# Optimization experiments

Hardware: AMD Instinct MI355X
Metric: run time of the kernel (lower is better)

The kernel has to match this reference:

```python
import jax, jax.numpy as jnp
import numpy as np

NUM_CLUSTERS = 5000  # labels.max()+1, fixed statically for jit
B, K, D, N = 256, 64, 2048, 50000
NHID, H2, NCLASS = 512, 256, 2


def setup_inputs() -> dict:
    key = jax.random.key(0)
    ks = jax.random.split(key, 16)
    s = lambda f_in: 1.0 / np.sqrt(f_in)
    return {
        "indexes": jax.random.randint(ks[0], (B,), 0, N),
        "features": jax.random.normal(ks[1], (N, D), dtype=jnp.float32),
        "labels": jax.random.randint(ks[2], (N,), 0, NUM_CLUSTERS),
        "domain": 1,
        "ori_0": 0,
        "ori_knn_neighbor": jax.random.randint(ks[3], (B, K), 0, N),
        "all_pred": jax.random.normal(ks[4], (B, K, NCLASS), dtype=jnp.float32),
        # GraphConv params (L-GCN style: weight [2*in, out])
        "W1": jax.random.normal(ks[5], (2 * D, NHID), jnp.float32) * s(2 * D),
        "b1": jnp.zeros((NHID,), jnp.float32),
        "W2": jax.random.normal(ks[6], (2 * NHID, H2), jnp.float32) * s(2 * NHID),
        "b2": jnp.zeros((H2,), jnp.float32),
        # classifier: Linear(256,256) -> PReLU(256) -> Linear(256,2)
        "Wc1": jax.random.normal(ks[7], (H2, H2), jnp.float32) * s(H2),
        "bc1": jnp.zeros((H2,), jnp.float32),
        "prelu_a": jnp.full((H2,), 0.25, jnp.float32),
        "Wc2": jax.random.normal(ks[8], (H2, NCLASS), jnp.float32) * s(H2),
        "bc2": jnp.zeros((NCLASS,), jnp.float32),
    }


def _gconv(x, A, W, b):
    # MeanAggregator: bmm(A, x); GraphConv: relu(cat([x, Ax]) @ W + b)
    agg = jnp.einsum('bkj,bjd->bkd', A, x)
    cat = jnp.concatenate([x, agg], axis=-1)
    return jax.nn.relu(jnp.einsum('bkd,df->bkf', cat, W) + b)


def reference(indexes, features, labels, domain, ori_0, ori_knn_neighbor, all_pred,
              W1, b1, W2, b2, Wc1, bc1, prelu_a, Wc2, bc2):
    # ---- cluster mean features (torch: index_add_ then divide; no_grad) ----
    clu_sum = jax.ops.segment_sum(features, labels, num_segments=NUM_CLUSTERS)
    nums = jax.ops.segment_sum(jnp.ones((features.shape[0],), features.dtype),
                               labels, num_segments=NUM_CLUSTERS)
    clu_mean = clu_sum / jnp.maximum(nums, 1.0)[:, None]  # [C, D]

    # ---- batched per-query subgraph construction (vectorized over B) ----
    clu_lab = labels[ori_knn_neighbor]            # [B, K]
    clu_feat = clu_mean[clu_lab]                  # [B, K, D]
    clu_feat = clu_feat.at[:, 0, :].set(features[indexes])  # pivot = raw feature

    A = jnp.einsum('bkd,bjd->bkj', clu_feat, clu_feat)       # pairwise similarity
    A = A * jnp.exp(all_pred[:, :, 1])[:, None, :]           # confidence weighting
    A = jax.nn.softmax(A, axis=-1)                           # row-normalized adjacency

    x = clu_feat / jnp.linalg.norm(clu_feat, axis=-1, keepdims=True)
    x = x - x[:, 0:1, :]                                     # center on pivot

    # (entire construction above is under torch.no_grad)
    x = jax.lax.stop_gradient(x)
    A = jax.lax.stop_gradient(A)

    # ---- GCN layers + classifier ----
    x = _gconv(x, A, W1, b1)      # [B, K, 512]
    x = _gconv(x, A, W2, b2)      # [B, K, 256]
    x0 = x.reshape(-1, H2)        # [B*K, 256]
    h = x0 @ Wc1 + bc1
    h = jnp.where(h >= 0, h, prelu_a * h)  # PReLU(256)
    logits = h @ Wc2 + bc2                 # [B*K, 2]

    # output_feat=True branch
    simm = jnp.sum(clu_mean * clu_mean, axis=1)                   # [C]
    pred = jax.nn.softmax(logits.reshape(B, K, NCLASS), axis=2)   # [B, K, 2]
    return (pred, simm)
```

## Files before the change

kernel.cpp:

```cpp
#include <hip/hip_runtime.h>
#include <math.h>

#define Bq 256
#define Kn 64
#define Dd 2048
#define Nn 50000
#define Cc 5000
#define NHID 512
#define H2d 256
#define LDH 264
#define MP 5376
#define PIVROW 5120

typedef __attribute__((ext_vector_type(8))) __bf16 bf16x8;
typedef __attribute__((ext_vector_type(4))) float f32x4;

__device__ __forceinline__ unsigned short f2bf(float f) {
    union { float f; unsigned int u; } v;
    v.f = f;
    unsigned int u = v.u;
    unsigned int r = (u + 0x7fff + ((u >> 16) & 1)) >> 16;
    return (unsigned short)r;
}
__device__ __forceinline__ float bf2f(unsigned short h) {
    union { unsigned int u; float f; } v;
    v.u = ((unsigned int)h) << 16;
    return v.f;
}

__global__ void k_zero_multi(int* __restrict__ p0, int n0,
                             int* __restrict__ p1, int n1,
                             int* __restrict__ p2, int n2,
                             int* __restrict__ p3, int n3) {
    int i = blockIdx.x * 256 + threadIdx.x;
    if (i < n0) { p0[i] = 0; return; }
    i -= n0;
    if (i < n1) { p1[i] = 0; return; }
    i -= n1;
    if (i < n2) { p2[i] = 0; return; }
    i -= n2;
    if (i < n3) p3[i] = 0;
}

__global__ void k_count(const int* __restrict__ labels, int* __restrict__ cnt, int n) {
    int i = blockIdx.x * 256 + threadIdx.x;
    if (i < n) atomicAdd(&cnt[labels[i]], 1);
}

__global__ void k_alloc(const int* __restrict__ cnt, int* __restrict__ off,
                        int* __restrict__ pos, int* __restrict__ total, int C) {
    int c = blockIdx.x * 256 + threadIdx.x;
    if (c < C) {
        int o = atomicAdd(total, cnt[c]);
        off[c] = o;
        pos[c] = o;
    }
}

__global__ void k_scatter(const int* __restrict__ labels, int* __restrict__ pos,
                          int* __restrict__ rowidx, int n) {
    int i = blockIdx.x * 256 + threadIdx.x;
    if (i < n) {
        int p = atomicAdd(&pos[labels[i]], 1);
        rowidx[p] = i;
    }
}

__global__ __launch_bounds__(256) void k_meansimm(
    const float* __restrict__ feat, const int* __restrict__ rowidx,
    const int* __restrict__ off, const int* __restrict__ cnt,
    const int* __restrict__ indexes,
    float* __restrict__ clu_mean, float* __restrict__ simm,
    unsigned short* __restrict__ PA) {
    int c = blockIdx.x;
    int t = threadIdx.x;
    __shared__ float red[256];

    if (c >= Cc) {
        int b = c - Cc;
        const float* row = feat + (size_t)indexes[b] * Dd;
        float4 v0 = *(const float4*)(row + t * 4);
        float4 v1 = *(const float4*)(row + 1024 + t * 4);
        float ss = v0.x * v0.x + v0.y * v0.y + v0.z * v0.z + v0.w * v0.w +
                   v1.x * v1.x + v1.y * v1.y + v1.z * v1.z + v1.w * v1.w;
        red[t] = ss;
        __syncthreads();
        for (int s2 = 128; s2 > 0; s2 >>= 1) {
            if (t < s2) red[t] += red[t + s2];
            __syncthreads();
        }
        float tot = red[0];
        float rnn = (tot > 0.f) ? rsqrtf(tot) : 0.f;
        ushort4 c0, c1;
        c0.x = f2bf(v0.x * rnn); c0.y = f2bf(v0.y * rnn);
        c0.z = f2bf(v0.z * rnn); c0.w = f2bf(v0.w * rnn);
        c1.x = f2bf(v1.x * rnn); c1.y = f2bf(v1.y * rnn);
        c1.z = f2bf(v1.z * rnn); c1.w = f2bf(v1.w * rnn);
        unsigned short* cr = PA + (size_t)(PIVROW + b) * Dd;
        *(ushort4*)(cr + t * 4) = c0;
        *(ushort4*)(cr + 1024 + t * 4) = c1;
        return;
    }

    int n = cnt[c], st = off[c];
    float4 a0 = {0.f, 0.f, 0.f, 0.f}, a1 = {0.f, 0.f, 0.f, 0.f};
    for (int r = 0; r < n; r++) {
        const float* row = feat + (size_t)rowidx[st + r] * Dd;
        float4 v0 = *(const float4*)(row + t * 4);
        float4 v1 = *(const float4*)(row + 1024 + t * 4);
        a0.x += v0.x; a0.y += v0.y; a0.z += v0.z; a0.w += v0.w;
        a1.x += v1.x; a1.y += v1.y; a1.z += v1.z; a1.w += v1.w;
    }
    float sc = 1.f / (float)(n > 1 ? n : 1);
    a0.x *= sc; a0.y *= sc; a0.z *= sc; a0.w *= sc;
    a1.x *= sc; a1.y *= sc; a1.z *= sc; a1.w *= sc;
    float* outr = clu_mean + (size_t)c * Dd;
    *(float4*)(outr + t * 4) = a0;
    *(float4*)(outr + 1024 + t * 4) = a1;
    float ss = a0.x * a0.x + a0.y * a0.y + a0.z * a0.z + a0.w * a0.w +
               a1.x * a1.x + a1.y * a1.y + a1.z * a1.z + a1.w * a1.w;
    red[t] = ss;
    __syncthreads();
    for (int s2 = 128; s2 > 0; s2 >>= 1) {
        if (t < s2) red[t] += red[t + s2];
        __syncthreads();
    }
    if (t == 0) simm[c] = red[0];
    float tot = red[0];
    float rnn = (tot > 0.f) ? rsqrtf(tot) : 0.f;
    ushort4 c0, c1;
    c0.x = f2bf(a0.x * rnn); c0.y = f2bf(a0.y * rnn);
    c0.z = f2bf(a0.z * rnn); c0.w = f2bf(a0.w * rnn);
    c1.x = f2bf(a1.x * rnn); c1.y = f2bf(a1.y * rnn);
    c1.z = f2bf(a1.z * rnn); c1.w = f2bf(a1.w * rnn);
    unsigned short* cr = PA + (size_t)c * Dd;
    *(ushort4*)(cr + t * 4) = c0;
    *(ushort4*)(cr + 1024 + t * 4) = c1;
}

__global__ __launch_bounds__(256) void k_build_ax(
    const float* __restrict__ feat, const float* __restrict__ clu_mean,
    const int* __restrict__ labels, const int* __restrict__ indexes,
    const int* __restrict__ knn, const float* __restrict__ all_pred,
    float* __restrict__ Abuf) {
    __shared__ unsigned short Hs[64 * LDH];
    __shared__ unsigned short Ls[64 * LDH];
    __shared__ float Gs[64 * 65];
    __shared__ const float* rowp[64];
    __shared__ float wj64[64];

    int b = blockIdx.x, tid = threadIdx.x;
    int wave = tid >> 6, lane = tid & 63, quad = lane >> 4, l16 = lane & 15;

    if (tid < 64) {
        const float* p = (tid == 0) ? feat + (size_t)indexes[b] * Dd
                                    : clu_mean + (size_t)labels[knn[b * 64 + tid]] * Dd;
        rowp[tid] = p;
        wj64[tid] = expf(all_pred[(b * 64 + tid) * 2 + 1]);
    }
    __syncthreads();

    f32x4 acc[4];
#pragma unroll
    for (int j = 0; j < 4; j++) acc[j] = (f32x4){0.f, 0.f, 0.f, 0.f};

    for (int ch = 0; ch < 8; ch++) {
        int d0 = ch * 256;
        __syncthreads();
#pragma unroll
        for (int q = 0; q < 16; q++) {
            int e4 = tid + q * 256;
            int row = e4 >> 6;
            int c4 = (e4 & 63) * 4;
            float4 v = *(const float4*)(rowp[row] + d0 + c4);
            ushort4 h, l;
            h.x = f2bf(v.x); l.x = f2bf(v.x - bf2f(h.x));
            h.y = f2bf(v.y); l.y = f2bf(v.y - bf2f(h.y));
            h.z = f2bf(v.z); l.z = f2bf(v.z - bf2f(h.z));
            h.w = f2bf(v.w); l.w = f2bf(v.w - bf2f(h.w));
            *(ushort4*)&Hs[row * LDH + c4] = h;
            *(ushort4*)&Ls[row * LDH + c4] = l;
        }
        __syncthreads();
#pragma unroll
        for (int ks = 0; ks < 8; ks++) {
            int kk = ks * 32 + quad * 8;
            bf16x8 ah = *(const bf16x8*)&Hs[(wave * 16 + l16) * LDH + kk];
            bf16x8 al = *(const bf16x8*)&Ls[(wave * 16 + l16) * LDH + kk];
#pragma unroll
            for (int j = 0; j < 4; j++) {
                bf16x8 bh = *(const bf16x8*)&Hs[(j * 16 + l16) * LDH + kk];
                bf16x8 bl = *(const bf16x8*)&Ls[(j * 16 + l16) * LDH + kk];
                acc[j] = __builtin_amdgcn_mfma_f32_16x16x32_bf16(ah, bh, acc[j], 0, 0, 0);
                acc[j] = __builtin_amdgcn_mfma_f32_16x16x32_bf16(ah, bl, acc[j], 0, 0, 0);
                acc[j] = __builtin_amdgcn_mfma_f32_16x16x32_bf16(al, bh, acc[j], 0, 0, 0);
            }
        }
    }
    __syncthreads();
#pragma unroll
    for (int j = 0; j < 4; j++)
#pragma unroll
        for (int r = 0; r < 4; r++)
            Gs[(wave * 16 + quad * 4 + r) * 65 + j * 16 + l16] = acc[j][r];
    __syncthreads();
    if (tid < 64) {
        int r = tid;
        float mx = -1e30f;
        for (int c = 0; c < 64; c++) {
            float v = Gs[r * 65 + c] * wj64[c];
            mx = fmaxf(mx, v);
        }
        float s = 0.f;
        for (int c = 0; c < 64; c++) {
            float e = expf(Gs[r * 65 + c] * wj64[c] - mx);
            Gs[r * 65 + c] = e;
            s += e;
        }
        float inv = 1.f / s;
        float* Arow = Abuf + ((size_t)b * 64 + r) * 64;
        for (int c = 0; c < 64; c++) Arow[c] = Gs[r * 65 + c] * inv;
    }
}

__device__ __forceinline__ void pack_item(const float* __restrict__ W,
                                          unsigned short* __restrict__ Bp,
                                          int K, int Nhalf, int split, int idx) {
    int Ntot = split ? 2 * Nhalf : Nhalf;
    int kb = idx / Ntot;
    int n = idx - kb * Ntot;
    float v[8];
#pragma unroll
    for (int j = 0; j < 8; j++) {
        int k = kb * 8 + j;
        if (split)
            v[j] = (n < Nhalf) ? W[(size_t)k * Nhalf + n]
                               : W[(size_t)(K + k) * Nhalf + (n - Nhalf)];
        else
            v[j] = W[(size_t)k * Nhalf + n];
    }
    ushort4 lo, hi;
    lo.x = f2bf(v[0]); lo.y = f2bf(v[1]); lo.z = f2bf(v[2]); lo.w = f2bf(v[3]);
    hi.x = f2bf(v[4]); hi.y = f2bf(v[5]); hi.z = f2bf(v[6]); hi.w = f2bf(v[7]);
    *(ushort4*)&Bp[(size_t)idx * 8] = lo;
    *(ushort4*)&Bp[(size_t)idx * 8 + 4] = hi;
}

__global__ __launch_bounds__(256) void k_pack_all(
    const float* __restrict__ W1, const float* __restrict__ W2,
    const float* __restrict__ Wc1, unsigned short* __restrict__ Bp1,
    unsigned short* __restrict__ Bp2, unsigned short* __restrict__ Bpc) {
    int blk = blockIdx.x;
    int tid = threadIdx.x;
    if (blk < 1024) {
        pack_item(W1, Bp1, Dd, NHID, 1, blk * 256 + tid);
    } else if (blk < 1024 + 128) {
        pack_item(W2, Bp2, 2 * NHID, H2d, 0, (blk - 1024) * 256 + tid);
    } else {
        pack_item(Wc1, Bpc, H2d, H2d, 0, (blk - 1152) * 256 + tid);
    }
}

template <int EPI>
__global__ __launch_bounds__(256) void gemm_bf16_mfma(
    const unsigned short* __restrict__ A, const unsigned short* __restrict__ Bp,
    void* __restrict__ Cout, int M, int K, int N,
    const float* __restrict__ bias, const float* __restrict__ pre_a,
    const float* __restrict__ wc2, float* __restrict__ lbuf) {
    __shared__ unsigned short Asm[128 * 32];
    __shared__ unsigned short Bsm[4 * 128 * 8];
    int tid = threadIdx.x;
    int wave = tid >> 6, lane = tid & 63;
    int quad = lane >> 4, l16 = lane & 15;
    int m0 = blockIdx.y * 128, n0 = blockIdx.x * 128;
    int wm = (wave >> 1) * 64, wn = (wave & 1) * 64;

    f32x4 acc[4][4];
#pragma unroll
    for (int i = 0; i < 4; i++)
#pragma unroll
        for (int j = 0; j < 4; j++) acc[i][j] = (f32x4){0.f, 0.f, 0.f, 0.f};

    int ia0 = wave * 2, ia1 = wave * 2 + 1;
    const unsigned short* gA0 = A + (size_t)(m0 + ia0 * 16 + (lane >> 2)) * K + (lane & 3) * 8;
    const unsigned short* gA1 = gA0 + (size_t)16 * K;
    const unsigned short* gB0 = Bp + (size_t)(n0 + lane) * 8 + (size_t)wave * N * 8;

    for (int k0 = 0; k0 < K; k0 += 32) {
        __syncthreads();
        size_t bko = (size_t)(k0 >> 3) * N * 8;
        __builtin_amdgcn_global_load_lds(
            (const __attribute__((address_space(1))) void*)(gA0 + k0),
            (__attribute__((address_space(3))) void*)(Asm + ia0 * 512), 16, 0, 0);
        __builtin_amdgcn_global_load_lds(
            (const __attribute__((address_space(1))) void*)(gA1 + k0),
            (__attribute__((address_space(3))) void*)(Asm + ia1 * 512), 16, 0, 0);
        __builtin_amdgcn_global_load_lds(
            (const __attribute__((address_space(1))) void*)(gB0 + bko),
            (__attribute__((address_space(3))) void*)(Bsm + wave * 1024), 16, 0, 0);
        __builtin_amdgcn_global_load_lds(
            (const __attribute__((address_space(1))) void*)(gB0 + bko + 512),
            (__attribute__((address_space(3))) void*)(Bsm + wave * 1024 + 512), 16, 0, 0);
        __syncthreads();

        bf16x8 a[4], b[4];
#pragma unroll
        for (int i = 0; i < 4; i++)
            a[i] = *(const bf16x8*)&Asm[(wm + i * 16 + l16) * 32 + quad * 8];
#pragma unroll
        for (int j = 0; j < 4; j++)
            b[j] = *(const bf16x8*)&Bsm[quad * 1024 + (wn + j * 16 + l16) * 8];
#pragma unroll
        for (int i = 0; i < 4; i++)
#pragma unroll
            for (int j = 0; j < 4; j++)
                acc[i][j] = __builtin_amdgcn_mfma_f32_16x16x32_bf16(
                    a[i], b[j], acc[i][j], 0, 0, 0);
    }

    if (EPI == 0) {
        float* C = (float*)Cout;
#pragma unroll
        for (int i = 0; i < 4; i++)
#pragma unroll
            for (int j = 0; j < 4; j++) {
                int col = n0 + wn + j * 16 + l16;
#pragma unroll
                for (int r = 0; r < 4; r++) {
                    int row = m0 + wm + i * 16 + quad * 4 + r;
                    C[(size_t)row * N + col] = acc[i][j][r];
                }
            }
    } else if (EPI == 2) {
        unsigned short* C = (unsigned short*)Cout;
#pragma unroll
        for (int i = 0; i < 4; i++)
#pragma unroll
            for (int j = 0; j < 4; j++) {
                int col = n0 + wn + j * 16 + l16;
                float bcol = bias[col];
#pragma unroll
                for (int r = 0; r < 4; r++) {
                    int row = m0 + wm + i * 16 + quad * 4 + r;
                    float v = acc[i][j][r] + bcol;
                    v = fmaxf(v, 0.f);
                    C[(size_t)row * N + col] = f2bf(v);
                }
            }
    } else {
#pragma unroll
        for (int i = 0; i < 4; i++) {
#pragma unroll
            for (int r = 0; r < 4; r++) {
                float l0 = 0.f, l1 = 0.f;
#pragma unroll
                for (int j = 0; j < 4; j++) {
                    int col = n0 + wn + j * 16 + l16;
                    float v = acc[i][j][r] + bias[col];
                    v = (v >= 0.f) ? v : pre_a[col] * v;
                    l0 += v * wc2[2 * col];
                    l1 += v * wc2[2 * col + 1];
                }
#pragma unroll
                for (int mm = 1; mm < 16; mm <<= 1) {
                    l0 += __shfl_xor(l0, mm, 64);
                    l1 += __shfl_xor(l1, mm, 64);
                }
                if (l16 == 0) {
                    int row = m0 + wm + i * 16 + quad * 4 + r;
                    atomicAdd(&lbuf[2 * row], l0);
                    atomicAdd(&lbuf[2 * row + 1], l1);
                }
            }
        }
    }
}

__global__ __launch_bounds__(256) void k_layer_agg1(
    const float* __restrict__ P, const float* __restrict__ Abuf,
    const int* __restrict__ labels, const int* __restrict__ knn,
    const float* __restrict__ bias, unsigned short* __restrict__ outp) {
    int b = blockIdx.x;
    int half = blockIdx.y;
    int tid = threadIdx.x;
    __shared__ float Ast[64 * 68];
    __shared__ float Us[64 * 68];
    __shared__ int rowid[64];
    int ty = tid >> 4, tx = tid & 15;
    if (tid < 64)
        rowid[tid] = (tid == 0) ? (PIVROW + b) : labels[knn[b * 64 + tid]];
    const float* Ab = Abuf + (size_t)b * 64 * 64;
    for (int e4 = tid; e4 < 1024; e4 += 256) {
        float4 v = *(const float4*)(Ab + e4 * 4);
        int row = e4 >> 4;
        int c4 = (e4 & 15) * 4;
        Ast[(c4 + 0) * 68 + row] = v.x;
        Ast[(c4 + 1) * 68 + row] = v.y;
        Ast[(c4 + 2) * 68 + row] = v.z;
        Ast[(c4 + 3) * 68 + row] = v.w;
    }
    const float* Q = P + (size_t)(PIVROW + b) * 1024;
    for (int n0 = half * (NHID / 2); n0 < (half + 1) * (NHID / 2); n0 += 64) {
        __syncthreads();
#pragma unroll
        for (int kq = 0; kq < 4; kq++) {
            int e4 = tid + kq * 256;
            int row = e4 >> 4;
            int c4 = (e4 & 15) * 4;
            float4 v = *(const float4*)(P + (size_t)rowid[row] * 1024 + NHID + n0 + c4);
            float4 q = *(const float4*)(Q + NHID + n0 + c4);
            v.x -= q.x; v.y -= q.y; v.z -= q.z; v.w -= q.w;
            *(float4*)&Us[row * 68 + c4] = v;
        }
        __syncthreads();
        float acc[4][4];
#pragma unroll
        for (int i = 0; i < 4; i++)
#pragma unroll
            for (int j = 0; j < 4; j++) acc[i][j] = 0.f;
        for (int kk = 0; kk < 64; kk++) {
            float4 a4 = *(const float4*)&Ast[kk * 68 + ty * 4];
            float4 b4 = *(const float4*)&Us[kk * 68 + tx * 4];
            float aa[4] = {a4.x, a4.y, a4.z, a4.w};
            float bb[4] = {b4.x, b4.y, b4.z, b4.w};
#pragma unroll
            for (int i = 0; i < 4; i++)
#pragma unroll
                for (int j = 0; j < 4; j++) acc[i][j] += aa[i] * bb[j];
        }
#pragma unroll
        for (int i = 0; i < 4; i++) {
            int krow = ty * 4 + i;
            int m = b * 64 + krow;
            int n = n0 + tx * 4;
            float4 ua = *(const float4*)(P + (size_t)rowid[krow] * 1024 + n);
            float4 qa = *(const float4*)(Q + n);
            float v0 = fmaxf(ua.x - qa.x + acc[i][0] + bias[n + 0], 0.f);
            float v1 = fmaxf(ua.y - qa.y + acc[i][1] + bias[n + 1], 0.f);
            float v2 = fmaxf(ua.z - qa.z + acc[i][2] + bias[n + 2], 0.f);
            float v3 = fmaxf(ua.w - qa.w + acc[i][3] + bias[n + 3], 0.f);
            ushort4 o_;
            o_.x = f2bf(v0); o_.y = f2bf(v1); o_.z = f2bf(v2); o_.w = f2bf(v3);
            *(ushort4*)(outp + (size_t)m * 1024 + n) = o_;
        }
        __syncthreads();
    }
}

__global__ __launch_bounds__(256) void k_premix(
    const unsigned short* __restrict__ xy1, const float* __restrict__ Abuf,
    unsigned short* __restrict__ yout) {
    int b = blockIdx.x;
    int half = blockIdx.y;
    int tid = threadIdx.x;
    __shared__ float Ast[64 * 68];
    __shared__ float Us[64 * 68];
    int ty = tid >> 4, tx = tid & 15;
    const float* Ab = Abuf + (size_t)b * 64 * 64;
    for (int e4 = tid; e4 < 1024; e4 += 256) {
        float4 v = *(const float4*)(Ab + e4 * 4);
        int row = e4 >> 4;
        int c4 = (e4 & 15) * 4;
        Ast[(c4 + 0) * 68 + row] = v.x;
        Ast[(c4 + 1) * 68 + row] = v.y;
        Ast[(c4 + 2) * 68 + row] = v.z;
        Ast[(c4 + 3) * 68 + row] = v.w;
    }
    for (int n0 = half * (NHID / 2); n0 < (half + 1) * (NHID / 2); n0 += 64) {
        __syncthreads();
#pragma unroll
        for (int kq = 0; kq < 4; kq++) {
            int e4 = tid + kq * 256;
            int row = e4 >> 4;
            int c4 = (e4 & 15) * 4;
            ushort4 u = *(const ushort4*)(xy1 + (size_t)(b * 64 + row) * 1024 + n0 + c4);
            Us[row * 68 + c4 + 0] = bf2f(u.x);
            Us[row * 68 + c4 + 1] = bf2f(u.y);
            Us[row * 68 + c4 + 2] = bf2f(u.z);
            Us[row * 68 + c4 + 3] = bf2f(u.w);
        }
        __syncthreads();
        float acc[4][4];
#pragma unroll
        for (int i = 0; i < 4; i++)
#pragma unroll
            for (int j = 0; j < 4; j++) acc[i][j] = 0.f;
        for (int kk = 0; kk < 64; kk++) {
            float4 a4 = *(const float4*)&Ast[kk * 68 + ty * 4];
            float4 b4 = *(const float4*)&Us[kk * 68 + tx * 4];
            float aa[4] = {a4.x, a4.y, a4.z, a4.w};
            float bb[4] = {b4.x, b4.y, b4.z, b4.w};
#pragma unroll
            for (int i = 0; i < 4; i++)
#pragma unroll
                for (int j = 0; j < 4; j++) acc[i][j] += aa[i] * bb[j];
        }
#pragma unroll
        for (int i = 0; i < 4; i++) {
            int m = b * 64 + ty * 4 + i;
            int n = n0 + tx * 4;
            ushort4 o_;
            o_.x = f2bf(acc[i][0]);
            o_.y = f2bf(acc[i][1]);
            o_.z = f2bf(acc[i][2]);
            o_.w = f2bf(acc[i][3]);
            *(ushort4*)(yout + (size_t)m * 1024 + 512 + n) = o_;
        }
        __syncthreads();
    }
}

__global__ void k_soft2(const float* __restrict__ lbuf, const float* __restrict__ bc2,
                        float* __restrict__ pred) {
    int m = blockIdx.x * 256 + threadIdx.x;
    if (m < Bq * Kn) {
        float L0 = lbuf[2 * m] + bc2[0];
        float L1 = lbuf[2 * m + 1] + bc2[1];
        float mx = fmaxf(L0, L1);
        float e0 = expf(L0 - mx), e1 = expf(L1 - mx);
        float inv = 1.f / (e0 + e1);
        pred[2 * m] = e0 * inv;
        pred[2 * m + 1] = e1 * inv;
    }
}

extern "C" void kernel_launch(void* const* d_in, const int* in_sizes, int n_in,
                              void* d_out, int out_size, void* d_ws, size_t ws_size,
                              hipStream_t stream) {
    const int* indexes = (const int*)d_in[0];
    const float* features = (const float*)d_in[1];
    const int* labels = (const int*)d_in[2];
    const int* knn = (const int*)d_in[5];
    const float* all_pred = (const float*)d_in[6];
    const float* W1 = (const float*)d_in[7];
    const float* b1 = (const float*)d_in[8];
    const float* W2 = (const float*)d_in[9];
    const float* b2 = (const float*)d_in[10];
    const float* Wc1 = (const float*)d_in[11];
    const float* bc1 = (const float*)d_in[12];
    const float* pre_a = (const float*)d_in[13];
    const float* Wc2 = (const float*)d_in[14];
    const float* bc2 = (const float*)d_in[15];
    float* out = (float*)d_out;

    char* w = (char*)d_ws;
    size_t o = 0;
    auto carve = [&](size_t bytes) -> char* {
        char* p = w + o;
        o += (bytes + 255) & ~(size_t)255;
        return p;
    };
    int* cnt = (int*)carve((size_t)Cc * 4);
    int* off = (int*)carve((size_t)Cc * 4);
    int* pos = (int*)carve((size_t)Cc * 4);
    int* total = (int*)carve(4);
    int* rowidx = (int*)carve((size_t)Nn * 4);
    float* clu_mean = (float*)carve((size_t)Cc * Dd * 4);
    unsigned short* PA = (unsigned short*)carve((size_t)MP * Dd * 2);
    float* Pout = (float*)carve((size_t)MP * 2 * NHID * 4);
    float* Abuf = (float*)carve((size_t)Bq * Kn * Kn * 4);
    unsigned short* Bp1 = (unsigned short*)carve((size_t)(Dd / 8) * 1024 * 8 * 2);
    unsigned short* xy1 = (unsigned short*)carve((size_t)Bq * Kn * 1024 * 2);
    unsigned short* Bp2 = (unsigned short*)carve((size_t)(2 * NHID / 8) * H2d * 8 * 2);
    unsigned short* x2 = (unsigned short*)carve((size_t)Bq * Kn * H2d * 2);
    unsigned short* Bpc = (unsigned short*)carve((size_t)(H2d / 8) * 256 * 8 * 2);
    float* lbuf = (float*)carve((size_t)Bq * Kn * 2 * 4);

    float* simm_out = out + (size_t)Bq * Kn * 2;

    {
        int nPad = (PIVROW - Cc) * Dd / 2;
        int nLb = Bq * Kn * 2;
        int ntot = Cc + nPad + nLb + 1;
        k_zero_multi<<<(ntot + 255) / 256, 256, 0, stream>>>(
            cnt, Cc, (int*)(PA + (size_t)Cc * Dd), nPad, (int*)lbuf, nLb, total, 1);
    }
    k_count<<<(Nn + 255) / 256, 256, 0, stream>>>(labels, cnt, Nn);
    k_alloc<<<(Cc + 255) / 256, 256, 0, stream>>>(cnt, off, pos, total, Cc);
    k_scatter<<<(Nn + 255) / 256, 256, 0, stream>>>(labels, pos, rowidx, Nn);

    k_meansimm<<<Cc + Bq, 256, 0, stream>>>(features, rowidx, off, cnt, indexes,
                                            clu_mean, simm_out, PA);

    k_build_ax<<<Bq, 256, 0, stream>>>(features, clu_mean, labels, indexes, knn,
                                       all_pred, Abuf);

    k_pack_all<<<1184, 256, 0, stream>>>(W1, W2, Wc1, Bp1, Bp2, Bpc);

    {
        dim3 g(1024 / 128, MP / 128);
        gemm_bf16_mfma<0><<<g, 256, 0, stream>>>(PA, Bp1, Pout, MP, Dd, 1024,
                                                 nullptr, nullptr, nullptr, nullptr);
    }
    {
        dim3 g(Bq, 2);
        k_layer_agg1<<<g, 256, 0, stream>>>(Pout, Abuf, labels, knn, b1, xy1);
    }
    {
        dim3 g(Bq, 2);
        k_premix<<<g, 256, 0, stream>>>(xy1, Abuf, xy1);
    }
    {
        dim3 g(H2d / 128, (Bq * Kn) / 128);
        gemm_bf16_mfma<2><<<g, 256, 0, stream>>>(xy1, Bp2, x2, Bq * Kn, 1024, H2d,
                                                 b2, nullptr, nullptr, nullptr);
    }
    {
        dim3 g(H2d / 128, (Bq * Kn) / 128);
        gemm_bf16_mfma<3><<<g, 256, 0, stream>>>(x2, Bpc, nullptr, Bq * Kn, H2d, H2d,
                                                 bc1, pre_a, Wc2, lbuf);
    }
    k_soft2<<<(Bq * Kn + 255) / 256, 256, 0, stream>>>(lbuf, bc2, out);

    (void)in_sizes; (void)n_in; (void)out_size; (void)ws_size;
}
```

Baseline: 829.7 us.

## Fuse GCN layer-1 aggregation and premix into one MFMA kernel; widen build_ax

Merges the first-layer aggregation kernel and the premix kernel into a single kernel. The A·U and A·x1 products now run on bf16 MFMA, with A and U split into hi/lo bf16 parts to keep accuracy close to fp32. This replaces the scalar fp32 FMA loops and avoids re-reading x1 from global memory. k_build_ax goes from 256 to 512 threads per block so the Gram MFMA work is shared across more waves, and its softmax is parallelised over 8 lanes per row using shuffles. The cost is more LDS traffic, transposed scalar LDS stores, and a small precision change in the A·x1 product, where only A is split into hi/lo.

```diff
diff --git a/kernel.cpp b/kernel.cpp
--- a/kernel.cpp
+++ b/kernel.cpp
@@ -11,6 +11,7 @@
 #define LDH 264
 #define MP 5376
 #define PIVROW 5120
+#define LDA1 72
 
 typedef __attribute__((ext_vector_type(8))) __bf16 bf16x8;
 typedef __attribute__((ext_vector_type(4))) float f32x4;
@@ -138,7 +139,7 @@
     *(ushort4*)(cr + 1024 + t * 4) = c1;
 }
 
-__global__ __launch_bounds__(256) void k_build_ax(
+__global__ __launch_bounds__(512) void k_build_ax(
     const float* __restrict__ feat, const float* __restrict__ clu_mean,
     const int* __restrict__ labels, const int* __restrict__ indexes,
     const int* __restrict__ knn, const float* __restrict__ all_pred,
@@ -151,6 +152,8 @@
 
     int b = blockIdx.x, tid = threadIdx.x;
     int wave = tid >> 6, lane = tid & 63, quad = lane >> 4, l16 = lane & 15;
+    int rs = (wave >> 1) * 16;
+    int cpair = (wave & 1) * 2;
 
     if (tid < 64) {
         const float* p = (tid == 0) ? feat + (size_t)indexes[b] * Dd
@@ -160,16 +163,16 @@
     }
     __syncthreads();
 
-    f32x4 acc[4];
-#pragma unroll
-    for (int j = 0; j < 4; j++) acc[j] = (f32x4){0.f, 0.f, 0.f, 0.f};
+    f32x4 acc[2];
+#pragma unroll
+    for (int j = 0; j < 2; j++) acc[j] = (f32x4){0.f, 0.f, 0.f, 0.f};
 
     for (int ch = 0; ch < 8; ch++) {
         int d0 = ch * 256;
         __syncthreads();
 #pragma unroll
-        for (int q = 0; q < 16; q++) {
-            int e4 = tid + q * 256;
+        for (int q = 0; q < 8; q++) {
+            int e4 = tid + q * 512;
             int row = e4 >> 6;
             int c4 = (e4 & 63) * 4;
             float4 v = *(const float4*)(rowp[row] + d0 + c4);
@@ -185,12 +188,13 @@
 #pragma unroll
         for (int ks = 0; ks < 8; ks++) {
             int kk = ks * 32 + quad * 8;
-            bf16x8 ah = *(const bf16x8*)&Hs[(wave * 16 + l16) * LDH + kk];
-            bf16x8 al = *(const bf16x8*)&Ls[(wave * 16 + l16) * LDH + kk];
-#pragma unroll
-            for (int j = 0; j < 4; j++) {
-                bf16x8 bh = *(const bf16x8*)&Hs[(j * 16 + l16) * LDH + kk];
-                bf16x8 bl = *(const bf16x8*)&Ls[(j * 16 + l16) * LDH + kk];
+            bf16x8 ah = *(const bf16x8*)&Hs[(rs + l16) * LDH + kk];
+            bf16x8 al = *(const bf16x8*)&Ls[(rs + l16) * LDH + kk];
+#pragma unroll
+            for (int j = 0; j < 2; j++) {
+                int jg = cpair + j;
+                bf16x8 bh = *(const bf16x8*)&Hs[(jg * 16 + l16) * LDH + kk];
+                bf16x8 bl = *(const bf16x8*)&Ls[(jg * 16 + l16) * LDH + kk];
                 acc[j] = __builtin_amdgcn_mfma_f32_16x16x32_bf16(ah, bh, acc[j], 0, 0, 0);
                 acc[j] = __builtin_amdgcn_mfma_f32_16x16x32_bf16(ah, bl, acc[j], 0, 0, 0);
                 acc[j] = __builtin_amdgcn_mfma_f32_16x16x32_bf16(al, bh, acc[j], 0, 0, 0);
@@ -199,27 +203,38 @@
     }
     __syncthreads();
 #pragma unroll
-    for (int j = 0; j < 4; j++)
+    for (int j = 0; j < 2; j++)
 #pragma unroll
         for (int r = 0; r < 4; r++)
-            Gs[(wave * 16 + quad * 4 + r) * 65 + j * 16 + l16] = acc[j][r];
+            Gs[(rs + quad * 4 + r) * 65 + (cpair + j) * 16 + l16] = acc[j][r];
     __syncthreads();
-    if (tid < 64) {
-        int r = tid;
+    {
+        int r = tid >> 3, s = tid & 7;
+        float e[8];
         float mx = -1e30f;
-        for (int c = 0; c < 64; c++) {
+#pragma unroll
+        for (int c8 = 0; c8 < 8; c8++) {
+            int c = s * 8 + c8;
             float v = Gs[r * 65 + c] * wj64[c];
+            e[c8] = v;
             mx = fmaxf(mx, v);
         }
-        float s = 0.f;
-        for (int c = 0; c < 64; c++) {
-            float e = expf(Gs[r * 65 + c] * wj64[c] - mx);
-            Gs[r * 65 + c] = e;
-            s += e;
-        }
-        float inv = 1.f / s;
+        mx = fmaxf(mx, __shfl_xor(mx, 1, 64));
+        mx = fmaxf(mx, __shfl_xor(mx, 2, 64));
+        mx = fmaxf(mx, __shfl_xor(mx, 4, 64));
+        float sum = 0.f;
+#pragma unroll
+        for (int c8 = 0; c8 < 8; c8++) {
+            e[c8] = expf(e[c8] - mx);
+            sum += e[c8];
+        }
+        sum += __shfl_xor(sum, 1, 64);
+        sum += __shfl_xor(sum, 2, 64);
+        sum += __shfl_xor(sum, 4, 64);
+        float inv = 1.f / sum;
         float* Arow = Abuf + ((size_t)b * 64 + r) * 64;
-        for (int c = 0; c < 64; c++) Arow[c] = Gs[r * 65 + c] * inv;
+#pragma unroll
+        for (int c8 = 0; c8 < 8; c8++) Arow[s * 8 + c8] = e[c8] * inv;
     }
 }
 
@@ -376,137 +391,116 @@
     }
 }
 
-__global__ __launch_bounds__(256) void k_layer_agg1(
+__global__ __launch_bounds__(256) void k_gcn1(
     const float* __restrict__ P, const float* __restrict__ Abuf,
     const int* __restrict__ labels, const int* __restrict__ knn,
-    const float* __restrict__ bias, unsigned short* __restrict__ outp) {
-    int b = blockIdx.x;
-    int half = blockIdx.y;
-    int tid = threadIdx.x;
-    __shared__ float Ast[64 * 68];
-    __shared__ float Us[64 * 68];
+    const float* __restrict__ bias, unsigned short* __restrict__ xy1) {
+    __shared__ unsigned short Ah[64 * LDA1], Al[64 * LDA1];
+    __shared__ unsigned short Xh[64 * LDA1], Xl[64 * LDA1];
+    __shared__ unsigned short Tt[64 * LDA1];
     __shared__ int rowid[64];
-    int ty = tid >> 4, tx = tid & 15;
+
+    int b = blockIdx.x, hf = blockIdx.y, tid = threadIdx.x;
+    int wave = tid >> 6, lane = tid & 63, quad = lane >> 4, l16 = lane & 15;
+
     if (tid < 64)
         rowid[tid] = (tid == 0) ? (PIVROW + b) : labels[knn[b * 64 + tid]];
+
     const float* Ab = Abuf + (size_t)b * 64 * 64;
-    for (int e4 = tid; e4 < 1024; e4 += 256) {
-        float4 v = *(const float4*)(Ab + e4 * 4);
+#pragma unroll
+    for (int q = 0; q < 4; q++) {
+        int e4 = tid + q * 256;
         int row = e4 >> 4;
         int c4 = (e4 & 15) * 4;
-        Ast[(c4 + 0) * 68 + row] = v.x;
-        Ast[(c4 + 1) * 68 + row] = v.y;
-        Ast[(c4 + 2) * 68 + row] = v.z;
-        Ast[(c4 + 3) * 68 + row] = v.w;
-    }
+        float4 v = *(const float4*)(Ab + row * 64 + c4);
+        ushort4 h, l;
+        h.x = f2bf(v.x); l.x = f2bf(v.x - bf2f(h.x));
+        h.y = f2bf(v.y); l.y = f2bf(v.y - bf2f(h.y));
+        h.z = f2bf(v.z); l.z = f2bf(v.z - bf2f(h.z));
+        h.w = f2bf(v.w); l.w = f2bf(v.w - bf2f(h.w));
+        *(ushort4*)&Ah[row * LDA1 + c4] = h;
+        *(ushort4*)&Al[row * LDA1 + c4] = l;
+    }
+
     const float* Q = P + (size_t)(PIVROW + b) * 1024;
-    for (int n0 = half * (NHID / 2); n0 < (half + 1) * (NHID / 2); n0 += 64) {
-        __syncthreads();
-#pragma unroll
-        for (int kq = 0; kq < 4; kq++) {
-            int e4 = tid + kq * 256;
-            int row = e4 >> 4;
+    unsigned short* xout = xy1 + (size_t)b * 64 * 1024;
+
+    for (int w = hf * 4; w < hf * 4 + 4; w++) {
+        int w0 = w * 64;
+        __syncthreads();
+#pragma unroll
+        for (int q = 0; q < 4; q++) {
+            int e4 = tid + q * 256;
+            int j = e4 >> 4;
             int c4 = (e4 & 15) * 4;
-            float4 v = *(const float4*)(P + (size_t)rowid[row] * 1024 + NHID + n0 + c4);
-            float4 q = *(const float4*)(Q + NHID + n0 + c4);
-            v.x -= q.x; v.y -= q.y; v.z -= q.z; v.w -= q.w;
-            *(float4*)&Us[row * 68 + c4] = v;
-        }
-        __syncthreads();
-        float acc[4][4];
-#pragma unroll
-        for (int i = 0; i < 4; i++)
-#pragma unroll
-            for (int j = 0; j < 4; j++) acc[i][j] = 0.f;
-        for (int kk = 0; kk < 64; kk++) {
-            float4 a4 = *(const float4*)&Ast[kk * 68 + ty * 4];
-            float4 b4 = *(const float4*)&Us[kk * 68 + tx * 4];
-            float aa[4] = {a4.x, a4.y, a4.z, a4.w};
-            float bb[4] = {b4.x, b4.y, b4.z, b4.w};
-#pragma unroll
-            for (int i = 0; i < 4; i++)
-#pragma unroll
-                for (int j = 0; j < 4; j++) acc[i][j] += aa[i] * bb[j];
-        }
-#pragma unroll
-        for (int i = 0; i < 4; i++) {
-            int krow = ty * 4 + i;
-            int m = b * 64 + krow;
-            int n = n0 + tx * 4;
-            float4 ua = *(const float4*)(P + (size_t)rowid[krow] * 1024 + n);
-            float4 qa = *(const float4*)(Q + n);
-            float v0 = fmaxf(ua.x - qa.x + acc[i][0] + bias[n + 0], 0.f);
-            float v1 = fmaxf(ua.y - qa.y + acc[i][1] + bias[n + 1], 0.f);
-            float v2 = fmaxf(ua.z - qa.z + acc[i][2] + bias[n + 2], 0.f);
-            float v3 = fmaxf(ua.w - qa.w + acc[i][3] + bias[n + 3], 0.f);
-            ushort4 o_;
-            o_.x = f2bf(v0); o_.y = f2bf(v1); o_.z = f2bf(v2); o_.w = f2bf(v3);
-            *(ushort4*)(outp + (size_t)m * 1024 + n) = o_;
-        }
-        __syncthreads();
-    }
-}
-
-__global__ __launch_bounds__(256) void k_premix(
-    const unsigned short* __restrict__ xy1, const float* __restrict__ Abuf,
-    unsigned short* __restrict__ yout) {
-    int b = blockIdx.x;
-    int half = blockIdx.y;
-    int tid = threadIdx.x;
-    __shared__ float Ast[64 * 68];
-    __shared__ float Us[64 * 68];
-    int ty = tid >> 4, tx = tid & 15;
-    const float* Ab = Abuf + (size_t)b * 64 * 64;
-    for (int e4 = tid; e4 < 1024; e4 += 256) {
-        float4 v = *(const float4*)(Ab + e4 * 4);
-        int row = e4 >> 4;
-        int c4 = (e4 & 15) * 4;
-        Ast[(c4 + 0) * 68 + row] = v.x;
-        Ast[(c4 + 1) * 68 + row] = v.y;
-        Ast[(c4 + 2) * 68 + row] = v.z;
-        Ast[(c4 + 3) * 68 + row] = v.w;
-    }
-    for (int n0 = half * (NHID / 2); n0 < (half + 1) * (NHID / 2); n0 += 64) {
-        __syncthreads();
-#pragma unroll
-        for (int kq = 0; kq < 4; kq++) {
-            int e4 = tid + kq * 256;
-            int row = e4 >> 4;
-            int c4 = (e4 & 15) * 4;
-            ushort4 u = *(const ushort4*)(xy1 + (size_t)(b * 64 + row) * 1024 + n0 + c4);
-            Us[row * 68 + c4 + 0] = bf2f(u.x);
-            Us[row * 68 + c4 + 1] = bf2f(u.y);
-            Us[row * 68 + c4 + 2] = bf2f(u.z);
-            Us[row * 68 + c4 + 3] = bf2f(u.w);
-        }
-        __syncthreads();
-        float acc[4][4];
-#pragma unroll
-        for (int i = 0; i < 4; i++)
-#pragma unroll
-            for (int j = 0; j < 4; j++) acc[i][j] = 0.f;
-        for (int kk = 0; kk < 64; kk++) {
-            float4 a4 = *(const float4*)&Ast[kk * 68 + ty * 4];
-            float4 b4 = *(const float4*)&Us[kk * 68 + tx * 4];
-            float aa[4] = {a4.x, a4.y, a4.z, a4.w};
-            float bb[4] = {b4.x, b4.y, b4.z, b4.w};
-#pragma unroll
-            for (int i = 0; i < 4; i++)
-#pragma unroll
-                for (int j = 0; j < 4; j++) acc[i][j] += aa[i] * bb[j];
-        }
-#pragma unroll
-        for (int i = 0; i < 4; i++) {
-            int m = b * 64 + ty * 4 + i;
-            int n = n0 + tx * 4;
-            ushort4 o_;
-            o_.x = f2bf(acc[i][0]);
-            o_.y = f2bf(acc[i][1]);
-            o_.z = f2bf(acc[i][2]);
-            o_.w = f2bf(acc[i][3]);
-            *(ushort4*)(yout + (size_t)m * 1024 + 512 + n) = o_;
-        }
-        __syncthreads();
+            float4 v = *(const float4*)(P + (size_t)rowid[j] * 1024 + 512 + w0 + c4);
+            float4 qv = *(const float4*)(Q + 512 + w0 + c4);
+            v.x -= qv.x; v.y -= qv.y; v.z -= qv.z; v.w -= qv.w;
+            unsigned short h;
+            h = f2bf(v.x); Xh[(c4 + 0) * LDA1 + j] = h; Xl[(c4 + 0) * LDA1 + j] = f2bf(v.x - bf2f(h));
+            h = f2bf(v.y); Xh[(c4 + 1) * LDA1 + j] = h; Xl[(c4 + 1) * LDA1 + j] = f2bf(v.y - bf2f(h));
+            h = f2bf(v.z); Xh[(c4 + 2) * LDA1 + j] = h; Xl[(c4 + 2) * LDA1 + j] = f2bf(v.z - bf2f(h));
+            h = f2bf(v.w); Xh[(c4 + 3) * LDA1 + j] = h; Xl[(c4 + 3) * LDA1 + j] = f2bf(v.w - bf2f(h));
+        }
+        __syncthreads();
+        f32x4 acc[4];
+#pragma unroll
+        for (int t = 0; t < 4; t++) acc[t] = (f32x4){0.f, 0.f, 0.f, 0.f};
+#pragma unroll
+        for (int ks = 0; ks < 2; ks++) {
+            int j0 = ks * 32 + quad * 8;
+            bf16x8 ah = *(const bf16x8*)&Ah[(wave * 16 + l16) * LDA1 + j0];
+            bf16x8 al = *(const bf16x8*)&Al[(wave * 16 + l16) * LDA1 + j0];
+#pragma unroll
+            for (int t = 0; t < 4; t++) {
+                bf16x8 bh = *(const bf16x8*)&Xh[(t * 16 + l16) * LDA1 + j0];
+                bf16x8 bl = *(const bf16x8*)&Xl[(t * 16 + l16) * LDA1 + j0];
+                acc[t] = __builtin_amdgcn_mfma_f32_16x16x32_bf16(ah, bh, acc[t], 0, 0, 0);
+                acc[t] = __builtin_amdgcn_mfma_f32_16x16x32_bf16(ah, bl, acc[t], 0, 0, 0);
+                acc[t] = __builtin_amdgcn_mfma_f32_16x16x32_bf16(al, bh, acc[t], 0, 0, 0);
+            }
+        }
+#pragma unroll
+        for (int t = 0; t < 4; t++) {
+            int cl = t * 16 + l16;
+            int c = w0 + cl;
+            float bb = bias[c];
+            float qa = Q[c];
+#pragma unroll
+            for (int r = 0; r < 4; r++) {
+                int k = wave * 16 + quad * 4 + r;
+                float ua = P[(size_t)rowid[k] * 1024 + c] - qa;
+                float v = fmaxf(acc[t][r] + ua + bb, 0.f);
+                unsigned short hv = f2bf(v);
+                xout[(size_t)k * 1024 + c] = hv;
+                Tt[cl * LDA1 + k] = hv;
+            }
+        }
+        __syncthreads();
+        f32x4 acc2[4];
+#pragma unroll
+        for (int t = 0; t < 4; t++) acc2[t] = (f32x4){0.f, 0.f, 0.f, 0.f};
+#pragma unroll
+        for (int ks = 0; ks < 2; ks++) {
+            int j0 = ks * 32 + quad * 8;
+            bf16x8 ah = *(const bf16x8*)&Ah[(wave * 16 + l16) * LDA1 + j0];
+            bf16x8 al = *(const bf16x8*)&Al[(wave * 16 + l16) * LDA1 + j0];
+#pragma unroll
+            for (int t = 0; t < 4; t++) {
+                bf16x8 bh = *(const bf16x8*)&Tt[(t * 16 + l16) * LDA1 + j0];
+                acc2[t] = __builtin_amdgcn_mfma_f32_16x16x32_bf16(ah, bh, acc2[t], 0, 0, 0);
+                acc2[t] = __builtin_amdgcn_mfma_f32_16x16x32_bf16(al, bh, acc2[t], 0, 0, 0);
+            }
+        }
+#pragma unroll
+        for (int t = 0; t < 4; t++) {
+            int c = 512 + w0 + t * 16 + l16;
+#pragma unroll
+            for (int r = 0; r < 4; r++) {
+                int k = wave * 16 + quad * 4 + r;
+                xout[(size_t)k * 1024 + c] = f2bf(acc2[t][r]);
+            }
+        }
     }
 }
 
@@ -582,7 +576,7 @@
     k_meansimm<<<Cc + Bq, 256, 0, stream>>>(features, rowidx, off, cnt, indexes,
                                             clu_mean, simm_out, PA);
 
-    k_build_ax<<<Bq, 256, 0, stream>>>(features, clu_mean, labels, indexes, knn,
+    k_build_ax<<<Bq, 512, 0, stream>>>(features, clu_mean, labels, indexes, knn,
                                        all_pred, Abuf);
 
     k_pack_all<<<1184, 256, 0, stream>>>(W1, W2, Wc1, Bp1, Bp2, Bpc);
@@ -594,11 +588,7 @@
     }
     {
         dim3 g(Bq, 2);
-        k_layer_agg1<<<g, 256, 0, stream>>>(Pout, Abuf, labels, knn, b1, xy1);
-    }
-    {
-        dim3 g(Bq, 2);
-        k_premix<<<g, 256, 0, stream>>>(xy1, Abuf, xy1);
+        k_gcn1<<<g, 256, 0, stream>>>(Pout, Abuf, labels, knn, b1, xy1);
     }
     {
         dim3 g(H2d / 128, (Bq * Kn) / 128);
```

New measurement: 798.0 us. 3.8% less time.
